# Kernel optimization log

Hardware: AMD Instinct MI355X
Metric: run time of the kernel (lower is better)

## Reference

```python
import jax, jax.numpy as jnp
import numpy as np

H = 128      # hidden_size
V = 32000    # vocab_size
B = 64       # batch
S = 128      # seq_len
EOS = 2
EPS = 1e-12


def setup_inputs() -> dict:
    key = jax.random.key(0)
    k1, k2, k3, k4 = jax.random.split(key, 4)
    input_ids = jax.random.randint(k1, (B, S), 0, V)
    # replicate SOHMM.__init__ (sep_token_id=None branch)
    alpha_exp = jax.nn.softmax(jax.random.normal(k2, (H, H, H)), axis=2)
    alpha_exp = alpha_exp.at[:, -1, :].set(1e-10).at[:, -1, -1].set(1.0)
    beta = jax.nn.log_softmax(jax.random.normal(k3, (H, V)), axis=1)
    beta = beta.at[-1, EOS].set(1e10).at[:-1, EOS].set(-1e10)
    beta = jax.nn.log_softmax(beta, axis=-1)
    gamma = jax.nn.log_softmax(jax.random.normal(k4, (H, H)).reshape(-1)).reshape(H, H)
    return {"input_ids": input_ids, "alpha_exp": alpha_exp, "beta": beta, "gamma": gamma}


def reference(input_ids, alpha_exp, beta, gamma):
    """Faithful jax port of SOHMM.forward. Returns (ys_stacked [S,H,H,B], y_final [B]).
    ys_stacked[t] corresponds to the list entry appended at time step S-1-t... i.e. ys in
    the same order as the torch list (first entry = t=S-1, last = t=0)."""
    batch, seq_len = input_ids.shape
    gamma_exp = jax.nn.softmax(gamma.reshape(-1)).reshape(gamma.shape)
    ids = input_ids.T  # [S, B]
    # input_probs[t, h, b] = beta[h, ids[t, b]], masked where id == -1
    input_probs = jnp.transpose(beta[:, ids], (1, 0, 2))  # [S, H, B]
    input_probs = jnp.where((ids != -1)[:, None, :], input_probs, 0.0)

    # t = S-1 step: y = 0 + input_probs[S-1] broadcast over leading H
    y0 = jnp.zeros((alpha_exp.shape[0],) + input_probs.shape[1:][::1][-2:][:0], dtype=input_probs.dtype)  # placeholder
    y0 = jnp.broadcast_to(input_probs[seq_len - 1][None], (alpha_exp.shape[0],) + input_probs[seq_len - 1].shape)

    def step(y, ip_t):
        # numerically-stable log-space second-order transition
        y_max = y.max(axis=(0, 1), keepdims=True)          # [1,1,B]
        y_exp = jnp.exp(y - y_max)
        y_new = jnp.einsum('ijk,jkb->ijb', alpha_exp, y_exp)
        y_new = jnp.log(y_new + EPS) + y_max
        y_new = y_new + ip_t[None]
        return y_new, y_new

    ips = input_probs[seq_len - 2::-1]  # t = S-2 down to 0
    y_last, ys_rest = jax.lax.scan(step, y0, ips)
    ys = jnp.concatenate([y0[None], ys_rest], axis=0)  # [S, H, H, B]

    y_max = y_last.max(axis=(0, 1))  # [B]
    y_final = jnp.log(jnp.einsum('ij,ijb->b', gamma_exp, jnp.exp(y_last - y_max[None, None])) + EPS) + y_max
    return ys, y_final
```

## Files before the change

kernel.cpp:

```cpp
#include <hip/hip_runtime.h>


#define Hd 128
#define Bd 64
#define Sd 128
#define Vd 32000
#define HBc (Hd * Bd)
#define HHBc (Hd * Hd * Bd)
#define NBLK 256
#define NTHR 1024
#define EPSF 1e-12f
#define FTAG 200u
#define SLOTW ((size_t)NBLK * Bd)

typedef __attribute__((ext_vector_type(4))) float f32x4;
typedef __attribute__((ext_vector_type(8))) short s16x8;
typedef __attribute__((ext_vector_type(4))) short s16x4;

__device__ __forceinline__ short f2bf(float f) {
  unsigned u = __builtin_bit_cast(unsigned, f);
  unsigned r = (u + 0x7fffu + ((u >> 16) & 1u)) >> 16;
  return (short)(r & 0xffffu);
}
__device__ __forceinline__ unsigned mono_enc(float f) {
  unsigned u = __builtin_bit_cast(unsigned, f);
  return u ^ ((u & 0x80000000u) ? 0xFFFFFFFFu : 0x80000000u);
}
__device__ __forceinline__ float mono_dec(unsigned m) {
  unsigned u = (m & 0x80000000u) ? (m ^ 0x80000000u) : ~m;
  return __builtin_bit_cast(float, u);
}
__device__ __forceinline__ unsigned packM(float f, unsigned tag) {
  return (tag << 24) | (mono_enc(f) >> 8);
}
__device__ __forceinline__ float decM(unsigned w) {
  return mono_dec((w & 0x00FFFFFFu) << 8);
}
__device__ __forceinline__ unsigned pack_y(float v, unsigned tag) {
  unsigned u = __builtin_bit_cast(unsigned, v);
  return ((u + 0x80u) & 0xFFFFFF00u) | tag;
}
__device__ __forceinline__ float as_f(unsigned u) { return __builtin_bit_cast(float, u); }
__device__ __forceinline__ unsigned pack24(float f, unsigned tag) {
  unsigned u = __builtin_bit_cast(unsigned, f);
  return ((u + 0x80u) & 0xFFFFFF00u) | tag;
}
__device__ __forceinline__ float dec24(unsigned v) {
  return __builtin_bit_cast(float, v & 0xFFFFFF00u);
}

__device__ __forceinline__ unsigned ld_u32(const unsigned* p) {
  return __hip_atomic_load(p, __ATOMIC_RELAXED, __HIP_MEMORY_SCOPE_AGENT);
}
__device__ __forceinline__ void st_u32(unsigned* p, unsigned v) {
  __hip_atomic_store(p, v, __ATOMIC_RELAXED, __HIP_MEMORY_SCOPE_AGENT);
}

__global__ __launch_bounds__(NTHR) void sohmm_persistent(
    const int* __restrict__ ids, const float* __restrict__ alpha,
    const float* __restrict__ beta, const float* __restrict__ gamma,
    float* __restrict__ out, unsigned* __restrict__ mslot,
    unsigned* __restrict__ fpart) {
  const int tid = threadIdx.x;
  const int bid = blockIdx.x;
  const int j = bid >> 1;
  const int ih = bid & 1;
  const int lane = tid & 63;
  const int w = tid >> 6;
  const int l15 = lane & 15;
  const int g4 = lane >> 4;
  const int wi = w >> 2;
  const int wb = w & 3;
  const int ti0 = ih * 64 + wi * 16;
  const int tb0 = wb * 16;
  const int bepi = tb0 + l15;
  const int sb = tid & 63;
  const int sq = tid >> 6;

  __shared__ __align__(16) short ET[64][132];
  __shared__ __align__(16) float ip_all[Sd][Bd];
  __shared__ float redM[16][64];
  __shared__ unsigned redSu[16][64];
  __shared__ float redF[16][64];
  __shared__ float wred[4][64];
  __shared__ float gex[128];

  s16x8 afrag[4];
  {
    const int i = ti0 + l15;
    const float* ap = alpha + ((size_t)i * Hd + j) * Hd;
#pragma unroll
    for (int kc = 0; kc < 4; ++kc) {
      const int k = kc * 32 + g4 * 8;
      f32x4 a0 = *(const f32x4*)(ap + k);
      f32x4 a1 = *(const f32x4*)(ap + k + 4);
      s16x8 f;
      f[0] = f2bf(a0[0]); f[1] = f2bf(a0[1]); f[2] = f2bf(a0[2]); f[3] = f2bf(a0[3]);
      f[4] = f2bf(a1[0]); f[5] = f2bf(a1[1]); f[6] = f2bf(a1[2]); f[7] = f2bf(a1[3]);
      afrag[kc] = f;
    }
  }

  for (int idx = tid; idx < Sd * Bd; idx += NTHR) {
    const int t = idx >> 6, b = idx & 63;
    ip_all[t][b] = beta[(size_t)j * Vd + ids[b * Sd + (Sd - 1 - t)]];
  }
  {
    float m = -3.4e38f;
#pragma unroll
    for (int c = 0; c < 4; ++c) {
      f32x4 g = *(const f32x4*)(gamma + (size_t)(c * NTHR + tid) * 4);
      m = fmaxf(fmaxf(fmaxf(m, g[0]), g[1]), fmaxf(g[2], g[3]));
    }
#pragma unroll
    for (int o = 32; o >= 1; o >>= 1) m = fmaxf(m, __shfl_xor(m, o, 64));
    if (lane == 0) redF[0][w] = m;
  }
  __syncthreads();
  {
    const int r = tid >> 4;
    const int b4 = (tid & 15) * 4;
    unsigned* yw = (unsigned*)out + (size_t)((ih * 64 + r) * Hd + j) * Bd + b4;
#pragma unroll
    for (int e = 0; e < 4; ++e) st_u32(yw + e, pack_y(ip_all[0][b4 + e], 1u));
  }
  {
    float gm = redF[0][0];
#pragma unroll
    for (int q = 1; q < 16; ++q) gm = fmaxf(gm, redF[0][q]);
    float ss = 0.f;
#pragma unroll
    for (int c = 0; c < 4; ++c) {
      f32x4 g = *(const f32x4*)(gamma + (size_t)(c * NTHR + tid) * 4);
      ss += __expf(g[0] - gm) + __expf(g[1] - gm) + __expf(g[2] - gm) + __expf(g[3] - gm);
    }
#pragma unroll
    for (int o = 32; o >= 1; o >>= 1) ss += __shfl_xor(ss, o, 64);
    if (lane == 0) redF[1][w] = ss;
    __syncthreads();
    float gs = 0.f;
#pragma unroll
    for (int q = 0; q < 16; ++q) gs += redF[1][q];
    if (tid < 128) gex[tid] = __expf(gamma[(size_t)tid * Hd + j] - gm) * (1.f / gs);
  }
  __syncthreads();

  float val[4];
#pragma unroll 1
  for (int s = 1; s < Sd; ++s) {
    const unsigned ytag = (unsigned)(2 * s - 1);
    const unsigned wtag = (unsigned)(2 * s + 1);

    const int k0 = sq * 8;
    const unsigned* ypw = (const unsigned*)out + (size_t)(s - 1) * HHBc + (size_t)j * HBc + sb;
    unsigned g[8];
#pragma unroll
    for (int e = 0; e < 8; ++e) g[e] = ld_u32(ypw + (size_t)(k0 + e) * Bd);
    {
      unsigned spins = 0;
      for (;;) {
        unsigned bad = 0;
#pragma unroll
        for (int e = 0; e < 8; ++e) bad |= (g[e] & 0xFFu) ^ ytag;
        if (!bad) break;
        if (++spins > (1u << 18)) break;
        __builtin_amdgcn_s_sleep(1);
#pragma unroll
        for (int e = 0; e < 8; ++e)
          if ((g[e] & 0xFFu) != ytag) g[e] = ld_u32(ypw + (size_t)(k0 + e) * Bd);
      }
    }

    {
      float pm = as_f(g[0]);
#pragma unroll
      for (int e = 1; e < 8; ++e) pm = fmaxf(pm, as_f(g[e]));
      redM[sq][sb] = pm;
    }
    __syncthreads();

    float Mst = redM[0][sb];
#pragma unroll
    for (int q = 1; q < 16; ++q) Mst = fmaxf(Mst, redM[q][sb]);
    float Me = redM[0][bepi];
#pragma unroll
    for (int q = 1; q < 16; ++q) Me = fmaxf(Me, redM[q][bepi]);
    const float add = Me + ip_all[s][bepi];

    {
      union { s16x8 v; } u;
#pragma unroll
      for (int e = 0; e < 8; ++e)
        ((short*)&u.v)[e] = f2bf(__expf(as_f(g[e]) - Mst));
      *(s16x8*)&ET[sb][k0] = u.v;
    }
    __syncthreads();

    f32x4 acc = (f32x4){0.f, 0.f, 0.f, 0.f};
#pragma unroll
    for (int kc = 0; kc < 4; ++kc) {
      const int kk = kc * 32 + g4 * 8;
      union { s16x4 h[2]; s16x8 v; } u;
      u.h[0] = *(const s16x4*)&ET[bepi][kk];
      u.h[1] = *(const s16x4*)&ET[bepi][kk + 4];
      acc = __builtin_amdgcn_mfma_f32_16x16x32_bf16(afrag[kc], u.v, acc, 0, 0, 0);
    }

    {
      unsigned* ycw = (unsigned*)out + (size_t)s * HHBc;
#pragma unroll
      for (int r = 0; r < 4; ++r) {
        float vv = __logf(acc[r] + EPSF) + add;
        val[r] = vv;
        st_u32(ycw + (size_t)(ti0 + g4 * 4 + r) * HBc + j * Bd + bepi, pack_y(vv, wtag));
      }
    }
  }

  {
    float mx = fmaxf(fmaxf(val[0], val[1]), fmaxf(val[2], val[3]));
    mx = fmaxf(mx, __shfl_xor(mx, 16, 64));
    mx = fmaxf(mx, __shfl_xor(mx, 32, 64));
    if (lane < 16) wred[wi][tb0 + lane] = mx;
  }
  __syncthreads();
  if (tid < 64) {
    float m = fmaxf(fmaxf(wred[0][tid], wred[1][tid]), fmaxf(wred[2][tid], wred[3][tid]));
    st_u32(mslot + (size_t)bid * Bd + tid, packM(m, 1u));
  }
  {
    const unsigned* pm = mslot + (size_t)(sq * 16) * Bd + sb;
    unsigned g2[16];
#pragma unroll
    for (int q = 0; q < 16; ++q) g2[q] = ld_u32(pm + (size_t)q * Bd);
    unsigned spins = 0;
    for (;;) {
      unsigned bad = 0;
#pragma unroll
      for (int q = 0; q < 16; ++q) bad |= (g2[q] >> 24) ^ 1u;
      if (!bad) break;
      if (++spins > (1u << 18)) break;
      __builtin_amdgcn_s_sleep(1);
#pragma unroll
      for (int q = 0; q < 16; ++q)
        if ((g2[q] >> 24) != 1u) g2[q] = ld_u32(pm + (size_t)q * Bd);
    }
    unsigned mx = 0u;
#pragma unroll
    for (int q = 0; q < 16; ++q) mx = g2[q] > mx ? g2[q] : mx;
    redSu[sq][sb] = mx;
  }
  __syncthreads();
  {
    unsigned mxe = 0u;
#pragma unroll
    for (int q = 0; q < 16; ++q) mxe = redSu[q][bepi] > mxe ? redSu[q][bepi] : mxe;
    const float M = decM(mxe);
    float sum = 0.f;
#pragma unroll
    for (int r = 0; r < 4; ++r)
      sum += gex[ti0 + g4 * 4 + r] * __expf(fminf(val[r] - M, 1.0f));
    sum += __shfl_xor(sum, 16, 64);
    sum += __shfl_xor(sum, 32, 64);
    if (lane < 16) wred[wi][tb0 + lane] = sum;
  }
  __syncthreads();
  if (tid < 64) {
    float sm = wred[0][tid] + wred[1][tid] + wred[2][tid] + wred[3][tid];
    st_u32(fpart + (size_t)bid * Bd + tid, pack24(sm, FTAG));
  }

  if (bid == 0) {
    const unsigned* pm = fpart + (size_t)(sq * 16) * Bd + sb;
    unsigned g[16];
#pragma unroll
    for (int q = 0; q < 16; ++q) g[q] = ld_u32(pm + (size_t)q * Bd);
    {
      unsigned spins = 0;
      for (;;) {
        unsigned bad = 0;
#pragma unroll
        for (int q = 0; q < 16; ++q) bad |= (g[q] & 0xFFu) ^ FTAG;
        if (!bad) break;
        if (++spins > (1u << 18)) break;
        __builtin_amdgcn_s_sleep(1);
#pragma unroll
        for (int q = 0; q < 16; ++q)
          if ((g[q] & 0xFFu) != FTAG) g[q] = ld_u32(pm + (size_t)q * Bd);
      }
    }
    float s16v = 0.f;
#pragma unroll
    for (int q = 0; q < 16; ++q) s16v += dec24(g[q]);
    redF[sq][sb] = s16v;
    __syncthreads();
    if (tid < 64) {
      unsigned mxe = 0u;
#pragma unroll
      for (int q = 0; q < 16; ++q) mxe = redSu[q][tid] > mxe ? redSu[q][tid] : mxe;
      float tot = 0.f;
#pragma unroll
      for (int q = 0; q < 16; ++q) tot += redF[q][tid];
      out[(size_t)Sd * HHBc + tid] = __logf(tot + EPSF) + decM(mxe);
    }
  }
}

extern "C" void kernel_launch(void* const* d_in, const int* in_sizes, int n_in,
                              void* d_out, int out_size, void* d_ws, size_t ws_size,
                              hipStream_t stream) {
  const int* ids = (const int*)d_in[0];
  const float* alpha = (const float*)d_in[1];
  const float* beta = (const float*)d_in[2];
  const float* gamma = (const float*)d_in[3];
  float* out = (float*)d_out;
  unsigned* mslot = (unsigned*)d_ws;
  unsigned* fpart = mslot + SLOTW;

  hipMemsetAsync(mslot, 0, 2 * SLOTW * sizeof(unsigned), stream);
  hipLaunchKernelGGL(sohmm_persistent, dim3(NBLK), dim3(NTHR), 0, stream,
                     ids, alpha, beta, gamma, out, mslot, fpart);
}
```

Baseline: 446.9 us.

## Repartition persistent blocks by batch half with per-column max and double-buffered LDS

Each block now owns one j and half of the batch, covering all 128 output rows, instead of half the rows and the full batch, and runs with 512 threads. The per-step max is taken per (j,b) with wave shuffles, which removes the cross-wave LDS reduction and one __syncthreads per time step. The exp tile and max buffer are double-buffered so only one barrier is needed per step. Each wave now issues two MFMAs per k-chunk. The trade-off is fewer threads to hide the latency of global polling, and a different exp normalisation (per-j column max rather than the global max) that could affect accuracy.

```diff
diff --git a/kernel.cpp b/kernel.cpp
--- a/kernel.cpp
+++ b/kernel.cpp
@@ -8,10 +8,9 @@
 #define HBc (Hd * Bd)
 #define HHBc (Hd * Hd * Bd)
 #define NBLK 256
-#define NTHR 1024
+#define NTHR 512
 #define EPSF 1e-12f
 #define FTAG 200u
-#define SLOTW ((size_t)NBLK * Bd)
 
 typedef __attribute__((ext_vector_type(4))) float f32x4;
 typedef __attribute__((ext_vector_type(8))) short s16x8;
@@ -64,30 +63,31 @@
   const int tid = threadIdx.x;
   const int bid = blockIdx.x;
   const int j = bid >> 1;
-  const int ih = bid & 1;
+  const int h = bid & 1;
   const int lane = tid & 63;
   const int w = tid >> 6;
   const int l15 = lane & 15;
   const int g4 = lane >> 4;
-  const int wi = w >> 2;
-  const int wb = w & 3;
-  const int ti0 = ih * 64 + wi * 16;
-  const int tb0 = wb * 16;
-  const int bepi = tb0 + l15;
-  const int sb = tid & 63;
-  const int sq = tid >> 6;
-
-  __shared__ __align__(16) short ET[64][132];
-  __shared__ __align__(16) float ip_all[Sd][Bd];
-  __shared__ float redM[16][64];
-  __shared__ unsigned redSu[16][64];
-  __shared__ float redF[16][64];
-  __shared__ float wred[4][64];
+  const int pb = w * 4 + (lane & 3);
+  const int kg = lane >> 2;
+  const int k0 = kg * 8;
+  const int i0 = w * 16;
+  const int bl0 = l15;
+  const int bl1 = 16 + l15;
+
+  __shared__ __align__(16) short ET[2][32][132];
+  __shared__ float MbL[2][32];
+  __shared__ __align__(16) float ipl[Sd][32];
   __shared__ float gex[128];
+  __shared__ float gred[2][8];
+  __shared__ float wredA[8][32];
+  __shared__ unsigned redSu[16][32];
+  __shared__ float redF2[8][64];
+  __shared__ unsigned redM2[8][64];
 
   s16x8 afrag[4];
   {
-    const int i = ti0 + l15;
+    const int i = i0 + l15;
     const float* ap = alpha + ((size_t)i * Hd + j) * Hd;
 #pragma unroll
     for (int kc = 0; kc < 4; ++kc) {
@@ -101,58 +101,59 @@
     }
   }
 
-  for (int idx = tid; idx < Sd * Bd; idx += NTHR) {
-    const int t = idx >> 6, b = idx & 63;
-    ip_all[t][b] = beta[(size_t)j * Vd + ids[b * Sd + (Sd - 1 - t)]];
+  for (int idx = tid; idx < Sd * 32; idx += NTHR) {
+    const int t = idx >> 5, bq = idx & 31;
+    ipl[t][bq] = beta[(size_t)j * Vd + ids[(h * 32 + bq) * Sd + (Sd - 1 - t)]];
   }
   {
     float m = -3.4e38f;
 #pragma unroll
-    for (int c = 0; c < 4; ++c) {
+    for (int c = 0; c < 8; ++c) {
       f32x4 g = *(const f32x4*)(gamma + (size_t)(c * NTHR + tid) * 4);
       m = fmaxf(fmaxf(fmaxf(m, g[0]), g[1]), fmaxf(g[2], g[3]));
     }
 #pragma unroll
     for (int o = 32; o >= 1; o >>= 1) m = fmaxf(m, __shfl_xor(m, o, 64));
-    if (lane == 0) redF[0][w] = m;
-  }
-  __syncthreads();
-  {
-    const int r = tid >> 4;
-    const int b4 = (tid & 15) * 4;
-    unsigned* yw = (unsigned*)out + (size_t)((ih * 64 + r) * Hd + j) * Bd + b4;
-#pragma unroll
-    for (int e = 0; e < 4; ++e) st_u32(yw + e, pack_y(ip_all[0][b4 + e], 1u));
-  }
-  {
-    float gm = redF[0][0];
-#pragma unroll
-    for (int q = 1; q < 16; ++q) gm = fmaxf(gm, redF[0][q]);
+    if (lane == 0) gred[0][w] = m;
+  }
+  __syncthreads();
+  {
+    const int i = tid >> 2;
+    const int b8 = (tid & 3) * 8;
+    unsigned* yw = (unsigned*)out + ((size_t)i * Hd + j) * Bd + h * 32 + b8;
+#pragma unroll
+    for (int e = 0; e < 8; ++e) st_u32(yw + e, pack_y(ipl[0][b8 + e], 1u));
+  }
+  {
+    float gm = gred[0][0];
+#pragma unroll
+    for (int q = 1; q < 8; ++q) gm = fmaxf(gm, gred[0][q]);
     float ss = 0.f;
 #pragma unroll
-    for (int c = 0; c < 4; ++c) {
+    for (int c = 0; c < 8; ++c) {
       f32x4 g = *(const f32x4*)(gamma + (size_t)(c * NTHR + tid) * 4);
       ss += __expf(g[0] - gm) + __expf(g[1] - gm) + __expf(g[2] - gm) + __expf(g[3] - gm);
     }
 #pragma unroll
     for (int o = 32; o >= 1; o >>= 1) ss += __shfl_xor(ss, o, 64);
-    if (lane == 0) redF[1][w] = ss;
+    if (lane == 0) gred[1][w] = ss;
     __syncthreads();
     float gs = 0.f;
 #pragma unroll
-    for (int q = 0; q < 16; ++q) gs += redF[1][q];
+    for (int q = 0; q < 8; ++q) gs += gred[1][q];
     if (tid < 128) gex[tid] = __expf(gamma[(size_t)tid * Hd + j] - gm) * (1.f / gs);
   }
   __syncthreads();
 
-  float val[4];
+  float val0[4], val1[4];
+  int p = 0;
 #pragma unroll 1
   for (int s = 1; s < Sd; ++s) {
     const unsigned ytag = (unsigned)(2 * s - 1);
     const unsigned wtag = (unsigned)(2 * s + 1);
 
-    const int k0 = sq * 8;
-    const unsigned* ypw = (const unsigned*)out + (size_t)(s - 1) * HHBc + (size_t)j * HBc + sb;
+    const unsigned* ypw = (const unsigned*)out + (size_t)(s - 1) * HHBc +
+                          (size_t)j * HBc + h * 32 + pb;
     unsigned g[8];
 #pragma unroll
     for (int e = 0; e < 8; ++e) g[e] = ld_u32(ypw + (size_t)(k0 + e) * Bd);
@@ -171,137 +172,166 @@
       }
     }
 
+    float pm = as_f(g[0]);
+#pragma unroll
+    for (int e = 1; e < 8; ++e) pm = fmaxf(pm, as_f(g[e]));
+    pm = fmaxf(pm, __shfl_xor(pm, 4, 64));
+    pm = fmaxf(pm, __shfl_xor(pm, 8, 64));
+    pm = fmaxf(pm, __shfl_xor(pm, 16, 64));
+    pm = fmaxf(pm, __shfl_xor(pm, 32, 64));
+
     {
-      float pm = as_f(g[0]);
-#pragma unroll
-      for (int e = 1; e < 8; ++e) pm = fmaxf(pm, as_f(g[e]));
-      redM[sq][sb] = pm;
+      s16x8 uv;
+#pragma unroll
+      for (int e = 0; e < 8; ++e) ((short*)&uv)[e] = f2bf(__expf(as_f(g[e]) - pm));
+      *(s16x8*)&ET[p][pb][k0] = uv;
+      if (kg == 0) MbL[p][pb] = pm;
     }
     __syncthreads();
 
-    float Mst = redM[0][sb];
-#pragma unroll
-    for (int q = 1; q < 16; ++q) Mst = fmaxf(Mst, redM[q][sb]);
-    float Me = redM[0][bepi];
-#pragma unroll
-    for (int q = 1; q < 16; ++q) Me = fmaxf(Me, redM[q][bepi]);
-    const float add = Me + ip_all[s][bepi];
-
-    {
-      union { s16x8 v; } u;
-#pragma unroll
-      for (int e = 0; e < 8; ++e)
-        ((short*)&u.v)[e] = f2bf(__expf(as_f(g[e]) - Mst));
-      *(s16x8*)&ET[sb][k0] = u.v;
-    }
-    __syncthreads();
-
-    f32x4 acc = (f32x4){0.f, 0.f, 0.f, 0.f};
+    f32x4 acc0 = (f32x4){0.f, 0.f, 0.f, 0.f};
+    f32x4 acc1 = (f32x4){0.f, 0.f, 0.f, 0.f};
 #pragma unroll
     for (int kc = 0; kc < 4; ++kc) {
       const int kk = kc * 32 + g4 * 8;
-      union { s16x4 h[2]; s16x8 v; } u;
-      u.h[0] = *(const s16x4*)&ET[bepi][kk];
-      u.h[1] = *(const s16x4*)&ET[bepi][kk + 4];
-      acc = __builtin_amdgcn_mfma_f32_16x16x32_bf16(afrag[kc], u.v, acc, 0, 0, 0);
+      union { s16x4 hh[2]; s16x8 v; } u0, u1;
+      u0.hh[0] = *(const s16x4*)&ET[p][bl0][kk];
+      u0.hh[1] = *(const s16x4*)&ET[p][bl0][kk + 4];
+      u1.hh[0] = *(const s16x4*)&ET[p][bl1][kk];
+      u1.hh[1] = *(const s16x4*)&ET[p][bl1][kk + 4];
+      acc0 = __builtin_amdgcn_mfma_f32_16x16x32_bf16(afrag[kc], u0.v, acc0, 0, 0, 0);
+      acc1 = __builtin_amdgcn_mfma_f32_16x16x32_bf16(afrag[kc], u1.v, acc1, 0, 0, 0);
     }
 
     {
+      const float add0 = MbL[p][bl0] + ipl[s][bl0];
+      const float add1 = MbL[p][bl1] + ipl[s][bl1];
       unsigned* ycw = (unsigned*)out + (size_t)s * HHBc;
 #pragma unroll
       for (int r = 0; r < 4; ++r) {
-        float vv = __logf(acc[r] + EPSF) + add;
-        val[r] = vv;
-        st_u32(ycw + (size_t)(ti0 + g4 * 4 + r) * HBc + j * Bd + bepi, pack_y(vv, wtag));
+        const size_t row = (size_t)(i0 + g4 * 4 + r) * HBc + (size_t)j * Bd + h * 32;
+        const float v0 = __logf(acc0[r] + EPSF) + add0;
+        const float v1 = __logf(acc1[r] + EPSF) + add1;
+        val0[r] = v0; val1[r] = v1;
+        st_u32(ycw + row + bl0, pack_y(v0, wtag));
+        st_u32(ycw + row + bl1, pack_y(v1, wtag));
       }
     }
-  }
-
-  {
-    float mx = fmaxf(fmaxf(val[0], val[1]), fmaxf(val[2], val[3]));
-    mx = fmaxf(mx, __shfl_xor(mx, 16, 64));
-    mx = fmaxf(mx, __shfl_xor(mx, 32, 64));
-    if (lane < 16) wred[wi][tb0 + lane] = mx;
-  }
-  __syncthreads();
-  if (tid < 64) {
-    float m = fmaxf(fmaxf(wred[0][tid], wred[1][tid]), fmaxf(wred[2][tid], wred[3][tid]));
-    st_u32(mslot + (size_t)bid * Bd + tid, packM(m, 1u));
-  }
-  {
-    const unsigned* pm = mslot + (size_t)(sq * 16) * Bd + sb;
-    unsigned g2[16];
-#pragma unroll
-    for (int q = 0; q < 16; ++q) g2[q] = ld_u32(pm + (size_t)q * Bd);
+    p ^= 1;
+  }
+
+  {
+    float m0 = fmaxf(fmaxf(val0[0], val0[1]), fmaxf(val0[2], val0[3]));
+    m0 = fmaxf(m0, __shfl_xor(m0, 16, 64));
+    m0 = fmaxf(m0, __shfl_xor(m0, 32, 64));
+    float m1 = fmaxf(fmaxf(val1[0], val1[1]), fmaxf(val1[2], val1[3]));
+    m1 = fmaxf(m1, __shfl_xor(m1, 16, 64));
+    m1 = fmaxf(m1, __shfl_xor(m1, 32, 64));
+    if (lane < 16) { wredA[w][lane] = m0; wredA[w][16 + lane] = m1; }
+  }
+  __syncthreads();
+  if (tid < 32) {
+    float mm = wredA[0][tid];
+#pragma unroll
+    for (int q = 1; q < 8; ++q) mm = fmaxf(mm, wredA[q][tid]);
+    st_u32(mslot + (size_t)j * Bd + h * 32 + tid, packM(mm, 1u));
+  }
+  {
+    const int b = tid & 31, jq = tid >> 5;
+    const unsigned* pm = mslot + (size_t)(jq * 8) * Bd + h * 32 + b;
+    unsigned gg[8];
+#pragma unroll
+    for (int q = 0; q < 8; ++q) gg[q] = ld_u32(pm + (size_t)q * Bd);
     unsigned spins = 0;
     for (;;) {
       unsigned bad = 0;
 #pragma unroll
-      for (int q = 0; q < 16; ++q) bad |= (g2[q] >> 24) ^ 1u;
+      for (int q = 0; q < 8; ++q) bad |= (gg[q] >> 24) ^ 1u;
       if (!bad) break;
       if (++spins > (1u << 18)) break;
       __builtin_amdgcn_s_sleep(1);
 #pragma unroll
-      for (int q = 0; q < 16; ++q)
-        if ((g2[q] >> 24) != 1u) g2[q] = ld_u32(pm + (size_t)q * Bd);
+      for (int q = 0; q < 8; ++q)
+        if ((gg[q] >> 24) != 1u) gg[q] = ld_u32(pm + (size_t)q * Bd);
     }
     unsigned mx = 0u;
 #pragma unroll
-    for (int q = 0; q < 16; ++q) mx = g2[q] > mx ? g2[q] : mx;
-    redSu[sq][sb] = mx;
-  }
-  __syncthreads();
-  {
-    unsigned mxe = 0u;
-#pragma unroll
-    for (int q = 0; q < 16; ++q) mxe = redSu[q][bepi] > mxe ? redSu[q][bepi] : mxe;
-    const float M = decM(mxe);
-    float sum = 0.f;
-#pragma unroll
-    for (int r = 0; r < 4; ++r)
-      sum += gex[ti0 + g4 * 4 + r] * __expf(fminf(val[r] - M, 1.0f));
-    sum += __shfl_xor(sum, 16, 64);
-    sum += __shfl_xor(sum, 32, 64);
-    if (lane < 16) wred[wi][tb0 + lane] = sum;
-  }
-  __syncthreads();
-  if (tid < 64) {
-    float sm = wred[0][tid] + wred[1][tid] + wred[2][tid] + wred[3][tid];
-    st_u32(fpart + (size_t)bid * Bd + tid, pack24(sm, FTAG));
+    for (int q = 0; q < 8; ++q) mx = gg[q] > mx ? gg[q] : mx;
+    redSu[jq][b] = mx;
+  }
+  __syncthreads();
+  {
+    unsigned mg0 = redSu[0][bl0], mg1 = redSu[0][bl1];
+#pragma unroll
+    for (int q = 1; q < 16; ++q) {
+      mg0 = redSu[q][bl0] > mg0 ? redSu[q][bl0] : mg0;
+      mg1 = redSu[q][bl1] > mg1 ? redSu[q][bl1] : mg1;
+    }
+    const float Mg0 = decM(mg0), Mg1 = decM(mg1);
+    float s0 = 0.f, s1 = 0.f;
+#pragma unroll
+    for (int r = 0; r < 4; ++r) {
+      const float gx = gex[i0 + g4 * 4 + r];
+      s0 += gx * __expf(val0[r] - Mg0);
+      s1 += gx * __expf(val1[r] - Mg1);
+    }
+    s0 += __shfl_xor(s0, 16, 64); s0 += __shfl_xor(s0, 32, 64);
+    s1 += __shfl_xor(s1, 16, 64); s1 += __shfl_xor(s1, 32, 64);
+    if (lane < 16) { wredA[w][lane] = s0; wredA[w][16 + lane] = s1; }
+  }
+  __syncthreads();
+  if (tid < 32) {
+    float tot = wredA[0][tid];
+#pragma unroll
+    for (int q = 1; q < 8; ++q) tot += wredA[q][tid];
+    st_u32(fpart + (size_t)j * Bd + h * 32 + tid, pack24(tot, FTAG));
   }
 
   if (bid == 0) {
-    const unsigned* pm = fpart + (size_t)(sq * 16) * Bd + sb;
-    unsigned g[16];
-#pragma unroll
-    for (int q = 0; q < 16; ++q) g[q] = ld_u32(pm + (size_t)q * Bd);
+    const int b = tid & 63, jq = tid >> 6;
+    const unsigned* pf = fpart + (size_t)(jq * 16) * Bd + b;
+    const unsigned* pmm = mslot + (size_t)(jq * 16) * Bd + b;
+    unsigned gf[16], gm[16];
+#pragma unroll
+    for (int q = 0; q < 16; ++q) { gf[q] = ld_u32(pf + (size_t)q * Bd); gm[q] = ld_u32(pmm + (size_t)q * Bd); }
     {
       unsigned spins = 0;
       for (;;) {
         unsigned bad = 0;
 #pragma unroll
-        for (int q = 0; q < 16; ++q) bad |= (g[q] & 0xFFu) ^ FTAG;
+        for (int q = 0; q < 16; ++q) {
+          bad |= (gf[q] & 0xFFu) ^ FTAG;
+          bad |= (gm[q] >> 24) ^ 1u;
+        }
         if (!bad) break;
         if (++spins > (1u << 18)) break;
         __builtin_amdgcn_s_sleep(1);
 #pragma unroll
-        for (int q = 0; q < 16; ++q)
-          if ((g[q] & 0xFFu) != FTAG) g[q] = ld_u32(pm + (size_t)q * Bd);
+        for (int q = 0; q < 16; ++q) {
+          if ((gf[q] & 0xFFu) != FTAG) gf[q] = ld_u32(pf + (size_t)q * Bd);
+          if ((gm[q] >> 24) != 1u) gm[q] = ld_u32(pmm + (size_t)q * Bd);
+        }
       }
     }
-    float s16v = 0.f;
-#pragma unroll
-    for (int q = 0; q < 16; ++q) s16v += dec24(g[q]);
-    redF[sq][sb] = s16v;
+    float sf = 0.f;
+    unsigned mx = 0u;
+#pragma unroll
+    for (int q = 0; q < 16; ++q) {
+      sf += dec24(gf[q]);
+      mx = gm[q] > mx ? gm[q] : mx;
+    }
+    redF2[jq][b] = sf;
+    redM2[jq][b] = mx;
     __syncthreads();
     if (tid < 64) {
-      unsigned mxe = 0u;
-#pragma unroll
-      for (int q = 0; q < 16; ++q) mxe = redSu[q][tid] > mxe ? redSu[q][tid] : mxe;
       float tot = 0.f;
-#pragma unroll
-      for (int q = 0; q < 16; ++q) tot += redF[q][tid];
-      out[(size_t)Sd * HHBc + tid] = __logf(tot + EPSF) + decM(mxe);
+      unsigned mg = 0u;
+#pragma unroll
+      for (int q = 0; q < 8; ++q) {
+        tot += redF2[q][tid];
+        mg = redM2[q][tid] > mg ? redM2[q][tid] : mg;
+      }
+      out[(size_t)Sd * HHBc + tid] = __logf(tot + EPSF) + decM(mg);
     }
   }
 }
@@ -315,9 +345,9 @@
   const float* gamma = (const float*)d_in[3];
   float* out = (float*)d_out;
   unsigned* mslot = (unsigned*)d_ws;
-  unsigned* fpart = mslot + SLOTW;
-
-  hipMemsetAsync(mslot, 0, 2 * SLOTW * sizeof(unsigned), stream);
+  unsigned* fpart = mslot + 128 * Bd;
+
+  hipMemsetAsync(mslot, 0, 2 * 128 * Bd * sizeof(unsigned), stream);
   hipLaunchKernelGGL(sohmm_persistent, dim3(NBLK), dim3(NTHR), 0, stream,
                      ids, alpha, beta, gamma, out, mslot, fpart);
 }
```

Measured after the change: 691.9 us. 54.8% more time.
